# Performance work log

Measured on AMD Instinct MI355X. Metric: run time of the kernel, lower is better.

## Reference

```python
import jax, jax.numpy as jnp
import numpy as np
from jax.ops import segment_sum

N_NODES = 50000
N_EDGES = 800000
N_GRAPHS = 256
F_IN, F_HID, N_HID, N_OUT = 64, 128, 512, 256


def setup_inputs() -> dict:
    key = jax.random.key(0)
    ks = jax.random.split(key, 12)
    x = jax.random.normal(ks[0], (N_NODES, F_IN), dtype=jnp.float32)
    edge_index = jax.random.randint(ks[1], (2, N_EDGES), 0, N_NODES, dtype=jnp.int64)
    batch = jnp.sort(jax.random.randint(ks[2], (N_NODES,), 0, N_GRAPHS, dtype=jnp.int64))
    def lin(k, fan_in, fan_out):
        s = 1.0 / np.sqrt(fan_in)
        return jax.random.uniform(k, (fan_in, fan_out), jnp.float32, -s, s)
    return {
        "x": x, "edge_index": edge_index, "batch": batch,
        "W0": lin(ks[3], F_IN, F_HID), "b0": jnp.zeros((F_HID,), jnp.float32),
        "W1": lin(ks[4], F_HID, F_HID), "b1": jnp.zeros((F_HID,), jnp.float32),
        "W2": lin(ks[5], F_HID, F_HID), "b2": jnp.zeros((F_HID,), jnp.float32),
        "Wm1": lin(ks[6], F_HID, N_HID), "bm1": jnp.zeros((N_HID,), jnp.float32),
        "Wm2": lin(ks[7], N_HID, N_OUT), "bm2": jnp.zeros((N_OUT,), jnp.float32),
    }


def _gcn_norm(edge_index, num_nodes):
    # PyG GCNConv default: add self-loops, symmetric D^{-1/2} A D^{-1/2} norm.
    loop = jnp.arange(num_nodes, dtype=edge_index.dtype)
    src = jnp.concatenate([edge_index[0], loop])
    dst = jnp.concatenate([edge_index[1], loop])
    deg = segment_sum(jnp.ones_like(src, dtype=jnp.float32), dst, num_segments=num_nodes)
    dis = jnp.where(deg > 0, jax.lax.rsqrt(jnp.maximum(deg, 1.0)), 0.0)
    norm = dis[src] * dis[dst]
    return src, dst, norm


def _gcn_conv(x, W, b, src, dst, norm, num_nodes):
    h = x @ W                                  # [N, F_out]
    msg = norm[:, None] * h[src]               # edge-wise gather  [E+N, F_out]
    out = segment_sum(msg, dst, num_segments=num_nodes)  # scatter-add
    return out + b


def reference(x, edge_index, batch, W0, b0, W1, b1, W2, b2, Wm1, bm1, Wm2, bm2):
    n = x.shape[0]
    src, dst, norm = _gcn_norm(edge_index, n)
    h = jax.nn.relu(_gcn_conv(x, W0, b0, src, dst, norm, n))
    h = jax.nn.relu(_gcn_conv(h, W1, b1, src, dst, norm, n))
    h = _gcn_conv(h, W2, b2, src, dst, norm, n)
    # global_mean_pool over graphs
    counts = segment_sum(jnp.ones((n,), jnp.float32), batch, num_segments=N_GRAPHS)
    g = segment_sum(h, batch, num_segments=N_GRAPHS) / jnp.maximum(counts, 1.0)[:, None]
    # mol_mlp: Linear -> ReLU -> Linear
    g = jax.nn.relu(g @ Wm1 + bm1)
    return g @ Wm2 + bm2
```

## Files before the change

kernel.cpp:

```cpp
#include <hip/hip_runtime.h>
#include <hip/hip_bf16.h>
#include <math.h>
#include <stdint.h>

#define N_NODES 50000
#define N_PAD   50048
#define N_EDGES 800000
#define N_GRAPHS 256
#define F_IN 64
#define F_HID 128
#define N_HID 512
#define N_OUT 256

#define NBKT   196
#define BKT_S  6144
#define BKT_CAP 8192
#define EPB    3328
#define NBIN_BLK ((N_EDGES + EPB - 1) / EPB)
#define DUMMY_NODE N_NODES

using bf16x8 = __attribute__((ext_vector_type(8))) short;
using f32x4  = __attribute__((ext_vector_type(4))) float;

__device__ __forceinline__ unsigned int bf16pair(float a, float b) {
    unsigned int ua = __float_as_uint(a);
    unsigned int ub = __float_as_uint(b);
    ua += 0x7fffu + ((ua >> 16) & 1u);
    ub += 0x7fffu + ((ub >> 16) & 1u);
    return (ua >> 16) | (ub & 0xffff0000u);
}
__device__ __forceinline__ unsigned short bf16one(float a) {
    unsigned int ua = __float_as_uint(a);
    ua += 0x7fffu + ((ua >> 16) & 1u);
    return (unsigned short)(ua >> 16);
}
__device__ __forceinline__ float bf16lo(unsigned int u) { return __uint_as_float(u << 16); }
__device__ __forceinline__ float bf16hi(unsigned int u) { return __uint_as_float(u & 0xffff0000u); }

__device__ __forceinline__ void acc8(float* a, uint4 r) {
    a[0] += bf16lo(r.x);  a[1] += bf16hi(r.x);
    a[2] += bf16lo(r.y);  a[3] += bf16hi(r.y);
    a[4] += bf16lo(r.z);  a[5] += bf16hi(r.z);
    a[6] += bf16lo(r.w);  a[7] += bf16hi(r.w);
}

__global__ void cvt_all(const float* __restrict__ in, const float* __restrict__ dis,
                        unsigned int* __restrict__ xb,
                        const float* __restrict__ W0, unsigned short* __restrict__ W0Tb,
                        const float* __restrict__ W1, unsigned short* __restrict__ W1Tb) {
    const int NX = N_NODES * F_IN / 4;
    int idx = blockIdx.x * blockDim.x + threadIdx.x;
    if (idx < NX) {
        int node = idx >> 4;
        float d = dis[node];
        float4 v = ((const float4*)in)[idx];
        ((uint2*)xb)[idx] = make_uint2(bf16pair(d * v.x, d * v.y),
                                       bf16pair(d * v.z, d * v.w));
        if (idx < 16)
            ((uint2*)xb)[(size_t)N_NODES * 16 + idx] = make_uint2(0u, 0u);
    } else {
        int j = idx - NX;
        const int N0 = F_IN * 128;
        const int N1 = F_HID * 128;
        if (j < N0) {
            int k = j >> 7, n = j & 127;
            W0Tb[n * F_IN + k] = bf16one(W0[j]);
        } else if (j < N0 + N1) {
            int jj = j - N0;
            int k = jj >> 7, n = jj & 127;
            W1Tb[n * F_HID + k] = bf16one(W1[jj]);
        }
    }
}

__global__ __launch_bounds__(256) void bin_edges(const int* __restrict__ ei,
                                                 int* __restrict__ bucketCur,
                                                 unsigned int* __restrict__ binned) {
    __shared__ int hist[NBKT];
    __shared__ int lbase[NBKT];
    __shared__ int lcur[NBKT];
    __shared__ int gbase[NBKT];
    __shared__ int scn[256];
    __shared__ unsigned int staging[EPB];
    int tid = threadIdx.x;
    int base = blockIdx.x * EPB;
    int cnt = N_EDGES - base; if (cnt > EPB) cnt = EPB;
    if (tid < NBKT) hist[tid] = 0;
    __syncthreads();
    unsigned int pk[13]; int nk = 0;
#pragma unroll
    for (int u = 0; u < 13; ++u) {
        int e = base + u * 256 + tid;
        if (u * 256 + tid < cnt) {
            unsigned int s = (unsigned int)ei[e];
            unsigned int d = (unsigned int)ei[N_EDGES + e];
            unsigned int b = d >> 8;
            pk[nk++] = (b << 24) | (s << 8) | (d & 255u);
        }
    }
    for (int u = 0; u < nk; ++u) atomicAdd(&hist[pk[u] >> 24], 1);
    __syncthreads();
    int h = (tid < NBKT) ? hist[tid] : 0;
    scn[tid] = h;
    __syncthreads();
    for (int off = 1; off < 256; off <<= 1) {
        int t = (tid >= off) ? scn[tid - off] : 0;
        __syncthreads();
        scn[tid] += t;
        __syncthreads();
    }
    if (tid < NBKT) { int e0 = scn[tid] - h; lbase[tid] = e0; lcur[tid] = e0; }
    __syncthreads();
    for (int u = 0; u < nk; ++u) {
        int pos = atomicAdd(&lcur[pk[u] >> 24], 1);
        staging[pos] = pk[u];
    }
    if (tid < NBKT && hist[tid] > 0)
        gbase[tid] = atomicAdd(&bucketCur[tid], hist[tid]);
    __syncthreads();
    for (int k = tid; k < cnt; k += 256) {
        unsigned int v = staging[k];
        int b = v >> 24;
        binned[(size_t)b * BKT_S + gbase[b] + (k - lbase[b])] = v & 0xffffffu;
    }
}

__global__ __launch_bounds__(256) void deg_scatter(const unsigned int* __restrict__ binned,
                                                   const int* __restrict__ bucketCur,
                                                   int* __restrict__ degs,
                                                   float* __restrict__ dis,
                                                   int* __restrict__ offsets,
                                                   unsigned short* __restrict__ csr) {
    __shared__ int hist[256];
    __shared__ int tsum[256];
    __shared__ int lcur[256];
    __shared__ uint4 scsr4[BKT_CAP / 8];
    unsigned short* scsr = (unsigned short*)scsr4;
    int b = blockIdx.x;
    int tid = threadIdx.x;
    int node0 = b << 8;
    hist[tid] = 0;
    __syncthreads();
    int cnt = bucketCur[b];
    const unsigned int* bb = &binned[(size_t)b * BKT_S];
    for (int k = tid; k < cnt; k += 256)
        atomicAdd(&hist[bb[k] & 255u], 1);
    __syncthreads();
    int d = hist[tid];
    int s = (d + 15) & ~15;
    tsum[tid] = s;
    __syncthreads();
    for (int off = 1; off < 256; off <<= 1) {
        int t = (tid >= off) ? tsum[tid - off] : 0;
        __syncthreads();
        tsum[tid] += t;
        __syncthreads();
    }
    int excl = tsum[tid] - s;
    int tot = tsum[255];
    int csrB = b * BKT_CAP;
    int node = node0 + tid;
    if (node < N_NODES) {
        degs[node] = d;
        dis[node] = rsqrtf((float)(d + 1));
        offsets[node] = csrB + excl;
    }
    lcur[tid] = excl;
    uint2 dv = make_uint2(0xC350C350u, 0xC350C350u);
    for (int k = tid; k < (tot >> 2); k += 256) ((uint2*)scsr)[k] = dv;
    __syncthreads();
    for (int k = tid; k < cnt; k += 256) {
        unsigned int v = bb[k];
        int dl = v & 255u;
        int p = atomicAdd(&lcur[dl], 1);
        scsr[p] = (unsigned short)(v >> 8);
    }
    __syncthreads();
    for (int k = tid; k < (tot >> 3); k += 256)
        ((uint4*)(csr + csrB))[k] = scsr4[k];
}

__global__ __launch_bounds__(256) void gemm01_mfma(const unsigned short* __restrict__ Ab,
                                                   const unsigned short* __restrict__ W0T,
                                                   const float* __restrict__ b0,
                                                   const unsigned short* __restrict__ W1T,
                                                   const float* __restrict__ disv,
                                                   unsigned int* __restrict__ outb, int M) {
    __shared__ unsigned short tile[4][16 * 128];
    int wv = threadIdx.x >> 6;
    int lane = threadIdx.x & 63;
    int m = lane & 15;
    int quad = lane >> 4;
    int row0 = blockIdx.x * 64 + wv * 16;
    char* tl = (char*)&tile[wv][0];
    f32x4 acc[8];
#pragma unroll
    for (int t = 0; t < 8; ++t) acc[t] = (f32x4){0.f, 0.f, 0.f, 0.f};
#pragma unroll
    for (int ks = 0; ks < F_IN; ks += 32) {
        bf16x8 af = *(const bf16x8*)&Ab[(size_t)(row0 + m) * F_IN + ks + quad * 8];
#pragma unroll
        for (int t = 0; t < 8; ++t) {
            bf16x8 bf = *(const bf16x8*)&W0T[(size_t)(t * 16 + m) * F_IN + ks + quad * 8];
            acc[t] = __builtin_amdgcn_mfma_f32_16x16x32_bf16(af, bf, acc[t], 0, 0, 0);
        }
    }
#pragma unroll
    for (int t = 0; t < 8; ++t) {
        int col = t * 16 + m;
        float bcol = b0[col];
#pragma unroll
        for (int r = 0; r < 4; ++r) {
            int row = quad * 4 + r;
            float v = fmaxf(acc[t][r] + bcol, 0.f);
            int byte = (row * 256 + col * 2) ^ ((row & 7) << 4);
            *(unsigned short*)(tl + byte) = bf16one(v);
        }
    }
    __syncthreads();
#pragma unroll
    for (int t = 0; t < 8; ++t) acc[t] = (f32x4){0.f, 0.f, 0.f, 0.f};
#pragma unroll
    for (int ks = 0; ks < F_HID; ks += 32) {
        int byte = (m * 256 + ks * 2 + quad * 16) ^ ((m & 7) << 4);
        bf16x8 af = *(const bf16x8*)(tl + byte);
#pragma unroll
        for (int t = 0; t < 8; ++t) {
            bf16x8 bf = *(const bf16x8*)&W1T[(size_t)(t * 16 + m) * F_HID + ks + quad * 8];
            acc[t] = __builtin_amdgcn_mfma_f32_16x16x32_bf16(af, bf, acc[t], 0, 0, 0);
        }
    }
    float dr[4];
#pragma unroll
    for (int r = 0; r < 4; ++r) {
        int row = row0 + quad * 4 + r;
        dr[r] = (row < M) ? disv[row] : 0.f;
    }
#pragma unroll
    for (int t = 0; t < 8; ++t) {
        int col = t * 16 + m;
#pragma unroll
        for (int r = 0; r < 4; ++r) {
            float v = acc[t][r] * dr[r];
            float vn = __shfl_xor(v, 1, 64);
            if ((m & 1) == 0) {
                int row = row0 + quad * 4 + r;
                outb[(size_t)row * 64 + (col >> 1)] = (row < M) ? bf16pair(v, vn) : 0u;
            }
        }
    }
}

template <bool RELU, bool BIAS, bool SCALEOUT>
__global__ __launch_bounds__(256) void aggregate128b(const uint4* __restrict__ hb4,
                                                     const int* __restrict__ offsets,
                                                     const int* __restrict__ degs,
                                                     const unsigned short* __restrict__ csr,
                                                     const float* __restrict__ dis,
                                                     const float* __restrict__ bias,
                                                     unsigned int* __restrict__ outb) {
    int wave = threadIdx.x >> 6;
    int lane = threadIdx.x & 63;
    int i = blockIdx.x * 4 + wave;
    int sub = lane >> 4;
    int q   = lane & 15;
    if (i >= N_NODES) {
        if (i == N_NODES && sub == 0)
            ((uint4*)outb)[(size_t)N_NODES * 16 + q] = make_uint4(0u, 0u, 0u, 0u);
        return;
    }
    float a[8];
#pragma unroll
    for (int k = 0; k < 8; ++k) a[k] = 0.f;
    int j = offsets[i];
    int e1 = j + ((degs[i] + 15) & ~15);
    for (; j < e1; j += 16) {
        uint2 w = *(const uint2*)&csr[j + 4 * sub];
        int s0 = w.x & 0xffff, s1 = w.x >> 16;
        int s2 = w.y & 0xffff, s3 = w.y >> 16;
        uint4 r0 = hb4[(size_t)s0 * 16 + q];
        uint4 r1 = hb4[(size_t)s1 * 16 + q];
        uint4 r2 = hb4[(size_t)s2 * 16 + q];
        uint4 r3 = hb4[(size_t)s3 * 16 + q];
        acc8(a, r0); acc8(a, r1); acc8(a, r2); acc8(a, r3);
    }
#pragma unroll
    for (int k = 0; k < 8; ++k) a[k] += __shfl_xor(a[k], 16, 64);
#pragma unroll
    for (int k = 0; k < 8; ++k) a[k] += __shfl_xor(a[k], 32, 64);
    uint4 su = hb4[(size_t)i * 16 + q];
    acc8(a, su);
    float dii = dis[i];
#pragma unroll
    for (int k = 0; k < 8; ++k) a[k] *= dii;
    if (BIAS) {
        float4 b0 = ((const float4*)bias)[2 * q];
        float4 b1 = ((const float4*)bias)[2 * q + 1];
        a[0] += b0.x; a[1] += b0.y; a[2] += b0.z; a[3] += b0.w;
        a[4] += b1.x; a[5] += b1.y; a[6] += b1.z; a[7] += b1.w;
    }
    if (RELU) {
#pragma unroll
        for (int k = 0; k < 8; ++k) a[k] = fmaxf(a[k], 0.f);
    }
    if (sub == 0) {
        float sc = SCALEOUT ? dii : 1.f;
        ((uint4*)outb)[(size_t)i * 16 + q] =
            make_uint4(bf16pair(sc * a[0], sc * a[1]), bf16pair(sc * a[2], sc * a[3]),
                       bf16pair(sc * a[4], sc * a[5]), bf16pair(sc * a[6], sc * a[7]));
    }
}

__global__ __launch_bounds__(256) void aggregate_xb(const uint4* __restrict__ xb4,
                                                    const float* __restrict__ x,
                                                    const int* __restrict__ offsets,
                                                    const int* __restrict__ degs,
                                                    const unsigned short* __restrict__ csr,
                                                    const float* __restrict__ dis,
                                                    unsigned int* __restrict__ outb) {
    int wave = threadIdx.x >> 6;
    int lane = threadIdx.x & 63;
    int i = blockIdx.x * 4 + wave;
    int sub = lane >> 3;
    int q   = lane & 7;
    if (i >= N_NODES) {
        if (i == N_NODES && sub == 0)
            ((uint4*)outb)[(size_t)N_NODES * 8 + q] = make_uint4(0u, 0u, 0u, 0u);
        return;
    }
    float a[8];
#pragma unroll
    for (int k = 0; k < 8; ++k) a[k] = 0.f;
    int j = offsets[i];
    int e1 = j + ((degs[i] + 15) & ~15);
    for (; j < e1; j += 16) {
        unsigned int w = *(const unsigned int*)&csr[j + 2 * sub];
        int s0 = w & 0xffff, s1 = w >> 16;
        uint4 r0 = xb4[(size_t)s0 * 8 + q];
        uint4 r1 = xb4[(size_t)s1 * 8 + q];
        acc8(a, r0); acc8(a, r1);
    }
#pragma unroll
    for (int k = 0; k < 8; ++k) a[k] += __shfl_xor(a[k], 8, 64);
#pragma unroll
    for (int k = 0; k < 8; ++k) a[k] += __shfl_xor(a[k], 16, 64);
#pragma unroll
    for (int k = 0; k < 8; ++k) a[k] += __shfl_xor(a[k], 32, 64);
    float dii = dis[i];
    float d2 = dii * dii;
    float4 sx0 = ((const float4*)x)[(size_t)i * 16 + 2 * q];
    float4 sx1 = ((const float4*)x)[(size_t)i * 16 + 2 * q + 1];
    a[0] = dii * a[0] + d2 * sx0.x;  a[1] = dii * a[1] + d2 * sx0.y;
    a[2] = dii * a[2] + d2 * sx0.z;  a[3] = dii * a[3] + d2 * sx0.w;
    a[4] = dii * a[4] + d2 * sx1.x;  a[5] = dii * a[5] + d2 * sx1.y;
    a[6] = dii * a[6] + d2 * sx1.z;  a[7] = dii * a[7] + d2 * sx1.w;
    if (sub == 0)
        ((uint4*)outb)[(size_t)i * 8 + q] =
            make_uint4(bf16pair(a[0], a[1]), bf16pair(a[2], a[3]),
                       bf16pair(a[4], a[5]), bf16pair(a[6], a[7]));
}

__global__ __launch_bounds__(256) void aggregate_pool(const uint4* __restrict__ hb4,
                                                      const int* __restrict__ offsets,
                                                      const int* __restrict__ degs,
                                                      const unsigned short* __restrict__ csr,
                                                      const float* __restrict__ dis,
                                                      const int* __restrict__ batch,
                                                      float* __restrict__ g_acc,
                                                      float* __restrict__ g_cnt) {
    __shared__ float pool[16][128];
    int tid = threadIdx.x;
    int grp = tid >> 4;
    int q   = tid & 15;
    int i = blockIdx.x * 16 + grp;
    float a[8];
#pragma unroll
    for (int k = 0; k < 8; ++k) a[k] = 0.f;
    if (i < N_NODES) {
        int j = offsets[i];
        int e1 = j + ((degs[i] + 15) & ~15);
        for (; j < e1; j += 16) {
            uint4 w0 = *(const uint4*)&csr[j];
            uint4 w1 = *(const uint4*)&csr[j + 8];
            int s[16];
            s[0] = w0.x & 0xffff;  s[1] = w0.x >> 16;
            s[2] = w0.y & 0xffff;  s[3] = w0.y >> 16;
            s[4] = w0.z & 0xffff;  s[5] = w0.z >> 16;
            s[6] = w0.w & 0xffff;  s[7] = w0.w >> 16;
            s[8] = w1.x & 0xffff;  s[9] = w1.x >> 16;
            s[10] = w1.y & 0xffff; s[11] = w1.y >> 16;
            s[12] = w1.z & 0xffff; s[13] = w1.z >> 16;
            s[14] = w1.w & 0xffff; s[15] = w1.w >> 16;
            uint4 r[8];
#pragma unroll
            for (int u = 0; u < 8; ++u) r[u] = hb4[(size_t)s[u] * 16 + q];
#pragma unroll
            for (int u = 0; u < 8; ++u) acc8(a, r[u]);
#pragma unroll
            for (int u = 0; u < 8; ++u) r[u] = hb4[(size_t)s[8 + u] * 16 + q];
#pragma unroll
            for (int u = 0; u < 8; ++u) acc8(a, r[u]);
        }
        uint4 su = hb4[(size_t)i * 16 + q];
        acc8(a, su);
        float dii = dis[i];
#pragma unroll
        for (int k = 0; k < 8; ++k) a[k] *= dii;
    }
#pragma unroll
    for (int k = 0; k < 8; ++k) pool[grp][k * 16 + q] = a[k];
    __syncthreads();
    if (tid < 128) {
        int f = tid;
        int lidx = (f & 7) * 16 + (f >> 3);
        int base = blockIdx.x * 16;
        float acc = 0.f; int cur = -1; float cnt = 0.f;
        for (int n = 0; n < 16; ++n) {
            int i2 = base + n;
            if (i2 >= N_NODES) break;
            int b = batch[i2];
            if (b != cur) {
                if (cur >= 0) {
                    atomicAdd(&g_acc[(size_t)cur * F_HID + f], acc);
                    if (f == 0) atomicAdd(&g_cnt[cur], cnt);
                }
                cur = b; acc = 0.f; cnt = 0.f;
            }
            acc += pool[n][lidx];
            cnt += 1.f;
        }
        if (cur >= 0) {
            atomicAdd(&g_acc[(size_t)cur * F_HID + f], acc);
            if (f == 0) atomicAdd(&g_cnt[cur], cnt);
        }
    }
}

__global__ __launch_bounds__(512) void fused_mlp(const float* __restrict__ g_acc,
                                                 const float* __restrict__ g_cnt,
                                                 const float* __restrict__ W2,
                                                 const float* __restrict__ b2,
                                                 const float* __restrict__ Wm1,
                                                 const float* __restrict__ bm1,
                                                 const float* __restrict__ Wm2,
                                                 const float* __restrict__ bm2,
                                                 float* __restrict__ out) {
    __shared__ float pool_row[F_HID];
    __shared__ float g2row[F_HID];
    __shared__ float hid[N_HID];
    int g = blockIdx.x;
    int t = threadIdx.x;
    if (t < F_HID) {
        float c = g_cnt[g];
        pool_row[t] = g_acc[(size_t)g * F_HID + t] / fmaxf(c, 1.0f);
    }
    __syncthreads();
    if (t < F_HID) {
        float acc = b2[t];
        for (int k = 0; k < F_HID; ++k) acc += pool_row[k] * W2[(size_t)k * F_HID + t];
        g2row[t] = acc;
    }
    __syncthreads();
    {
        float acc = bm1[t];
        for (int k = 0; k < F_HID; ++k) acc += g2row[k] * Wm1[(size_t)k * N_HID + t];
        hid[t] = fmaxf(acc, 0.f);
    }
    __syncthreads();
    if (t < N_OUT) {
        float acc = bm2[t];
        for (int k = 0; k < N_HID; ++k) acc += hid[k] * Wm2[(size_t)k * N_OUT + t];
        out[(size_t)g * N_OUT + t] = acc;
    }
}

extern "C" void kernel_launch(void* const* d_in, const int* in_sizes, int n_in,
                              void* d_out, int out_size, void* d_ws, size_t ws_size,
                              hipStream_t stream) {
    const float* x   = (const float*)d_in[0];
    const int* ei    = (const int*)d_in[1];
    const int* batch = (const int*)d_in[2];
    const float* W0 = (const float*)d_in[3];  const float* b0 = (const float*)d_in[4];
    const float* W1 = (const float*)d_in[5];  const float* b1 = (const float*)d_in[6];
    const float* W2 = (const float*)d_in[7];  const float* b2 = (const float*)d_in[8];
    const float* Wm1 = (const float*)d_in[9];  const float* bm1 = (const float*)d_in[10];
    const float* Wm2 = (const float*)d_in[11]; const float* bm2 = (const float*)d_in[12];

    char* p = (char*)d_ws;
    auto alloc = [&](size_t bytes) -> char* {
        char* r = p;
        p += (bytes + 255) & ~(size_t)255;
        return r;
    };
    int*   bucketCur = (int*)alloc(NBKT * 4);
    float* g_acc  = (float*)alloc((size_t)N_GRAPHS * F_HID * 4);
    float* g_cnt  = (float*)alloc(N_GRAPHS * 4);
    size_t zero_bytes = (size_t)(p - (char*)bucketCur);
    unsigned int* binned = (unsigned int*)alloc((size_t)NBKT * BKT_S * 4);
    int*   offsets = (int*)alloc((size_t)N_NODES * 4);
    int*   degs    = (int*)alloc((size_t)N_NODES * 4);
    float* dis     = (float*)alloc((size_t)N_NODES * 4);
    unsigned short* csr = (unsigned short*)alloc((size_t)NBKT * BKT_CAP * 2 + 32);
    unsigned int* xb     = (unsigned int*)alloc((size_t)N_PAD * F_IN / 2 * 4);
    unsigned int* axb    = (unsigned int*)alloc((size_t)N_PAD * F_IN / 2 * 4);
    unsigned int* h_tmpb = (unsigned int*)alloc((size_t)N_PAD * F_HID / 2 * 4);
    unsigned int* h_bb   = (unsigned int*)alloc((size_t)N_PAD * F_HID / 2 * 4);
    unsigned short* W0Tb = (unsigned short*)alloc((size_t)128 * F_IN * 2);
    unsigned short* W1Tb = (unsigned short*)alloc((size_t)128 * F_HID * 2);
    (void)ws_size; (void)in_sizes; (void)n_in; (void)out_size;

    (void)hipMemsetAsync(bucketCur, 0, zero_bytes, stream);

    bin_edges<<<NBIN_BLK, 256, 0, stream>>>(ei, bucketCur, binned);
    deg_scatter<<<NBKT, 256, 0, stream>>>(binned, bucketCur, degs, dis, offsets, csr);

    const int NCVT = N_NODES * F_IN / 4 + (F_IN + F_HID) * 128;
    cvt_all<<<(NCVT + 255) / 256, 256, 0, stream>>>(x, dis, xb, W0, W0Tb, W1, W1Tb);

    int agg_grid = N_NODES / 4 + 1;
    int mfma_grid = N_PAD / 64;

    aggregate_xb<<<agg_grid, 256, 0, stream>>>((const uint4*)xb, x, offsets, degs, csr, dis, axb);
    gemm01_mfma<<<mfma_grid, 256, 0, stream>>>(
        (const unsigned short*)axb, W0Tb, b0, W1Tb, dis, h_tmpb, N_NODES);
    aggregate128b<true, true, true><<<agg_grid, 256, 0, stream>>>(
        (const uint4*)h_tmpb, offsets, degs, csr, dis, b1, h_bb);
    aggregate_pool<<<(N_NODES + 15) / 16, 256, 0, stream>>>(
        (const uint4*)h_bb, offsets, degs, csr, dis, batch, g_acc, g_cnt);

    fused_mlp<<<N_GRAPHS, 512, 0, stream>>>(g_acc, g_cnt, W2, b2, Wm1, bm1, Wm2, bm2,
                                            (float*)d_out);
}
```

Measured before the change: 248.2 us.

## Fuse first-layer aggregation into MFMA GEMM and regroup aggregation threads per node

Layer-0 neighbor aggregation now runs inside the GEMM kernel. Each block aggregates its 64 rows into a swizzled LDS tile and feeds the MFMA directly, which removes the axb intermediate buffer and one launch. The 128-wide aggregation kernel now gives each node a 16-lane group that walks all 16 CSR entries per iteration, instead of splitting edges across a wave and reducing with shuffles. This trades cross-lane reductions for more serial gather work per thread. The fused kernel runs only 782 blocks, so the aggregation phase may have less parallelism to hide gather latency.

```diff
diff --git a/kernel.cpp b/kernel.cpp
--- a/kernel.cpp
+++ b/kernel.cpp
@@ -42,6 +42,19 @@
     a[2] += bf16lo(r.y);  a[3] += bf16hi(r.y);
     a[4] += bf16lo(r.z);  a[5] += bf16hi(r.z);
     a[6] += bf16lo(r.w);  a[7] += bf16hi(r.w);
+}
+
+__device__ __forceinline__ void csr16(const unsigned short* __restrict__ csr, int j, int* s) {
+    uint4 w0 = *(const uint4*)&csr[j];
+    uint4 w1 = *(const uint4*)&csr[j + 8];
+    s[0] = w0.x & 0xffff;  s[1] = w0.x >> 16;
+    s[2] = w0.y & 0xffff;  s[3] = w0.y >> 16;
+    s[4] = w0.z & 0xffff;  s[5] = w0.z >> 16;
+    s[6] = w0.w & 0xffff;  s[7] = w0.w >> 16;
+    s[8] = w1.x & 0xffff;  s[9] = w1.x >> 16;
+    s[10] = w1.y & 0xffff; s[11] = w1.y >> 16;
+    s[12] = w1.z & 0xffff; s[13] = w1.z >> 16;
+    s[14] = w1.w & 0xffff; s[15] = w1.w >> 16;
 }
 
 __global__ void cvt_all(const float* __restrict__ in, const float* __restrict__ dis,
@@ -180,25 +193,76 @@
         ((uint4*)(csr + csrB))[k] = scsr4[k];
 }
 
-__global__ __launch_bounds__(256) void gemm01_mfma(const unsigned short* __restrict__ Ab,
-                                                   const unsigned short* __restrict__ W0T,
-                                                   const float* __restrict__ b0,
-                                                   const unsigned short* __restrict__ W1T,
-                                                   const float* __restrict__ disv,
-                                                   unsigned int* __restrict__ outb, int M) {
+__global__ __launch_bounds__(256) void agg_gemm01(const uint4* __restrict__ xb4,
+                                                  const float* __restrict__ x,
+                                                  const int* __restrict__ offsets,
+                                                  const int* __restrict__ degs,
+                                                  const unsigned short* __restrict__ csr,
+                                                  const float* __restrict__ dis,
+                                                  const unsigned short* __restrict__ W0T,
+                                                  const float* __restrict__ b0,
+                                                  const unsigned short* __restrict__ W1T,
+                                                  unsigned int* __restrict__ outb, int M) {
+    __shared__ unsigned short atile[64 * 64];
     __shared__ unsigned short tile[4][16 * 128];
-    int wv = threadIdx.x >> 6;
-    int lane = threadIdx.x & 63;
+    int tid = threadIdx.x;
+    int row0 = blockIdx.x * 64;
+    char* at = (char*)atile;
+    {
+        int grp = tid >> 3;
+        int q   = tid & 7;
+#pragma unroll
+        for (int pass = 0; pass < 2; ++pass) {
+            int node = grp + pass * 32;
+            int i = row0 + node;
+            float a[8];
+#pragma unroll
+            for (int k = 0; k < 8; ++k) a[k] = 0.f;
+            if (i < N_NODES) {
+                int j = offsets[i];
+                int e1 = j + ((degs[i] + 15) & ~15);
+                for (; j < e1; j += 16) {
+                    int s[16];
+                    csr16(csr, j, s);
+                    uint4 r[8];
+#pragma unroll
+                    for (int u = 0; u < 8; ++u) r[u] = xb4[(size_t)s[u] * 8 + q];
+#pragma unroll
+                    for (int u = 0; u < 8; ++u) acc8(a, r[u]);
+#pragma unroll
+                    for (int u = 0; u < 8; ++u) r[u] = xb4[(size_t)s[8 + u] * 8 + q];
+#pragma unroll
+                    for (int u = 0; u < 8; ++u) acc8(a, r[u]);
+                }
+                float dii = dis[i];
+                float d2 = dii * dii;
+                float4 sx0 = ((const float4*)x)[(size_t)i * 16 + 2 * q];
+                float4 sx1 = ((const float4*)x)[(size_t)i * 16 + 2 * q + 1];
+                a[0] = dii * a[0] + d2 * sx0.x;  a[1] = dii * a[1] + d2 * sx0.y;
+                a[2] = dii * a[2] + d2 * sx0.z;  a[3] = dii * a[3] + d2 * sx0.w;
+                a[4] = dii * a[4] + d2 * sx1.x;  a[5] = dii * a[5] + d2 * sx1.y;
+                a[6] = dii * a[6] + d2 * sx1.z;  a[7] = dii * a[7] + d2 * sx1.w;
+            }
+            int byte = (node * 128 + q * 16) ^ ((node & 7) << 4);
+            *(uint4*)(at + byte) =
+                make_uint4(bf16pair(a[0], a[1]), bf16pair(a[2], a[3]),
+                           bf16pair(a[4], a[5]), bf16pair(a[6], a[7]));
+        }
+    }
+    __syncthreads();
+    int wv = tid >> 6;
+    int lane = tid & 63;
     int m = lane & 15;
     int quad = lane >> 4;
-    int row0 = blockIdx.x * 64 + wv * 16;
+    int wrow0 = row0 + wv * 16;
     char* tl = (char*)&tile[wv][0];
     f32x4 acc[8];
 #pragma unroll
     for (int t = 0; t < 8; ++t) acc[t] = (f32x4){0.f, 0.f, 0.f, 0.f};
 #pragma unroll
     for (int ks = 0; ks < F_IN; ks += 32) {
-        bf16x8 af = *(const bf16x8*)&Ab[(size_t)(row0 + m) * F_IN + ks + quad * 8];
+        int abyte = ((wv * 16 + m) * 128 + (ks + quad * 8) * 2) ^ ((m & 7) << 4);
+        bf16x8 af = *(const bf16x8*)(at + abyte);
 #pragma unroll
         for (int t = 0; t < 8; ++t) {
             bf16x8 bf = *(const bf16x8*)&W0T[(size_t)(t * 16 + m) * F_IN + ks + quad * 8];
@@ -233,8 +297,8 @@
     float dr[4];
 #pragma unroll
     for (int r = 0; r < 4; ++r) {
-        int row = row0 + quad * 4 + r;
-        dr[r] = (row < M) ? disv[row] : 0.f;
+        int row = wrow0 + quad * 4 + r;
+        dr[r] = (row < M) ? dis[row] : 0.f;
     }
 #pragma unroll
     for (int t = 0; t < 8; ++t) {
@@ -244,7 +308,7 @@
             float v = acc[t][r] * dr[r];
             float vn = __shfl_xor(v, 1, 64);
             if ((m & 1) == 0) {
-                int row = row0 + quad * 4 + r;
+                int row = wrow0 + quad * 4 + r;
                 outb[(size_t)row * 64 + (col >> 1)] = (row < M) ? bf16pair(v, vn) : 0u;
             }
         }
@@ -252,20 +316,19 @@
 }
 
 template <bool RELU, bool BIAS, bool SCALEOUT>
-__global__ __launch_bounds__(256) void aggregate128b(const uint4* __restrict__ hb4,
+__global__ __launch_bounds__(256) void aggregate128g(const uint4* __restrict__ hb4,
                                                      const int* __restrict__ offsets,
                                                      const int* __restrict__ degs,
                                                      const unsigned short* __restrict__ csr,
                                                      const float* __restrict__ dis,
                                                      const float* __restrict__ bias,
                                                      unsigned int* __restrict__ outb) {
-    int wave = threadIdx.x >> 6;
-    int lane = threadIdx.x & 63;
-    int i = blockIdx.x * 4 + wave;
-    int sub = lane >> 4;
-    int q   = lane & 15;
+    int tid = threadIdx.x;
+    int grp = tid >> 4;
+    int q   = tid & 15;
+    int i = blockIdx.x * 16 + grp;
     if (i >= N_NODES) {
-        if (i == N_NODES && sub == 0)
+        if (i == N_NODES)
             ((uint4*)outb)[(size_t)N_NODES * 16 + q] = make_uint4(0u, 0u, 0u, 0u);
         return;
     }
@@ -275,19 +338,18 @@
     int j = offsets[i];
     int e1 = j + ((degs[i] + 15) & ~15);
     for (; j < e1; j += 16) {
-        uint2 w = *(const uint2*)&csr[j + 4 * sub];
-        int s0 = w.x & 0xffff, s1 = w.x >> 16;
-        int s2 = w.y & 0xffff, s3 = w.y >> 16;
-        uint4 r0 = hb4[(size_t)s0 * 16 + q];
-        uint4 r1 = hb4[(size_t)s1 * 16 + q];
-        uint4 r2 = hb4[(size_t)s2 * 16 + q];
-        uint4 r3 = hb4[(size_t)s3 * 16 + q];
-        acc8(a, r0); acc8(a, r1); acc8(a, r2); acc8(a, r3);
-    }
-#pragma unroll
-    for (int k = 0; k < 8; ++k) a[k] += __shfl_xor(a[k], 16, 64);
-#pragma unroll
-    for (int k = 0; k < 8; ++k) a[k] += __shfl_xor(a[k], 32, 64);
+        int s[16];
+        csr16(csr, j, s);
+        uint4 r[8];
+#pragma unroll
+        for (int u = 0; u < 8; ++u) r[u] = hb4[(size_t)s[u] * 16 + q];
+#pragma unroll
+        for (int u = 0; u < 8; ++u) acc8(a, r[u]);
+#pragma unroll
+        for (int u = 0; u < 8; ++u) r[u] = hb4[(size_t)s[8 + u] * 16 + q];
+#pragma unroll
+        for (int u = 0; u < 8; ++u) acc8(a, r[u]);
+    }
     uint4 su = hb4[(size_t)i * 16 + q];
     acc8(a, su);
     float dii = dis[i];
@@ -303,61 +365,10 @@
 #pragma unroll
         for (int k = 0; k < 8; ++k) a[k] = fmaxf(a[k], 0.f);
     }
-    if (sub == 0) {
-        float sc = SCALEOUT ? dii : 1.f;
-        ((uint4*)outb)[(size_t)i * 16 + q] =
-            make_uint4(bf16pair(sc * a[0], sc * a[1]), bf16pair(sc * a[2], sc * a[3]),
-                       bf16pair(sc * a[4], sc * a[5]), bf16pair(sc * a[6], sc * a[7]));
-    }
-}
-
-__global__ __launch_bounds__(256) void aggregate_xb(const uint4* __restrict__ xb4,
-                                                    const float* __restrict__ x,
-                                                    const int* __restrict__ offsets,
-                                                    const int* __restrict__ degs,
-                                                    const unsigned short* __restrict__ csr,
-                                                    const float* __restrict__ dis,
-                                                    unsigned int* __restrict__ outb) {
-    int wave = threadIdx.x >> 6;
-    int lane = threadIdx.x & 63;
-    int i = blockIdx.x * 4 + wave;
-    int sub = lane >> 3;
-    int q   = lane & 7;
-    if (i >= N_NODES) {
-        if (i == N_NODES && sub == 0)
-            ((uint4*)outb)[(size_t)N_NODES * 8 + q] = make_uint4(0u, 0u, 0u, 0u);
-        return;
-    }
-    float a[8];
-#pragma unroll
-    for (int k = 0; k < 8; ++k) a[k] = 0.f;
-    int j = offsets[i];
-    int e1 = j + ((degs[i] + 15) & ~15);
-    for (; j < e1; j += 16) {
-        unsigned int w = *(const unsigned int*)&csr[j + 2 * sub];
-        int s0 = w & 0xffff, s1 = w >> 16;
-        uint4 r0 = xb4[(size_t)s0 * 8 + q];
-        uint4 r1 = xb4[(size_t)s1 * 8 + q];
-        acc8(a, r0); acc8(a, r1);
-    }
-#pragma unroll
-    for (int k = 0; k < 8; ++k) a[k] += __shfl_xor(a[k], 8, 64);
-#pragma unroll
-    for (int k = 0; k < 8; ++k) a[k] += __shfl_xor(a[k], 16, 64);
-#pragma unroll
-    for (int k = 0; k < 8; ++k) a[k] += __shfl_xor(a[k], 32, 64);
-    float dii = dis[i];
-    float d2 = dii * dii;
-    float4 sx0 = ((const float4*)x)[(size_t)i * 16 + 2 * q];
-    float4 sx1 = ((const float4*)x)[(size_t)i * 16 + 2 * q + 1];
-    a[0] = dii * a[0] + d2 * sx0.x;  a[1] = dii * a[1] + d2 * sx0.y;
-    a[2] = dii * a[2] + d2 * sx0.z;  a[3] = dii * a[3] + d2 * sx0.w;
-    a[4] = dii * a[4] + d2 * sx1.x;  a[5] = dii * a[5] + d2 * sx1.y;
-    a[6] = dii * a[6] + d2 * sx1.z;  a[7] = dii * a[7] + d2 * sx1.w;
-    if (sub == 0)
-        ((uint4*)outb)[(size_t)i * 8 + q] =
-            make_uint4(bf16pair(a[0], a[1]), bf16pair(a[2], a[3]),
-                       bf16pair(a[4], a[5]), bf16pair(a[6], a[7]));
+    float sc = SCALEOUT ? dii : 1.f;
+    ((uint4*)outb)[(size_t)i * 16 + q] =
+        make_uint4(bf16pair(sc * a[0], sc * a[1]), bf16pair(sc * a[2], sc * a[3]),
+                   bf16pair(sc * a[4], sc * a[5]), bf16pair(sc * a[6], sc * a[7]));
 }
 
 __global__ __launch_bounds__(256) void aggregate_pool(const uint4* __restrict__ hb4,
@@ -380,17 +391,8 @@
         int j = offsets[i];
         int e1 = j + ((degs[i] + 15) & ~15);
         for (; j < e1; j += 16) {
-            uint4 w0 = *(const uint4*)&csr[j];
-            uint4 w1 = *(const uint4*)&csr[j + 8];
             int s[16];
-            s[0] = w0.x & 0xffff;  s[1] = w0.x >> 16;
-            s[2] = w0.y & 0xffff;  s[3] = w0.y >> 16;
-            s[4] = w0.z & 0xffff;  s[5] = w0.z >> 16;
-            s[6] = w0.w & 0xffff;  s[7] = w0.w >> 16;
-            s[8] = w1.x & 0xffff;  s[9] = w1.x >> 16;
-            s[10] = w1.y & 0xffff; s[11] = w1.y >> 16;
-            s[12] = w1.z & 0xffff; s[13] = w1.z >> 16;
-            s[14] = w1.w & 0xffff; s[15] = w1.w >> 16;
+            csr16(csr, j, s);
             uint4 r[8];
 #pragma unroll
             for (int u = 0; u < 8; ++u) r[u] = hb4[(size_t)s[u] * 16 + q];
@@ -502,7 +504,6 @@
     float* dis     = (float*)alloc((size_t)N_NODES * 4);
     unsigned short* csr = (unsigned short*)alloc((size_t)NBKT * BKT_CAP * 2 + 32);
     unsigned int* xb     = (unsigned int*)alloc((size_t)N_PAD * F_IN / 2 * 4);
-    unsigned int* axb    = (unsigned int*)alloc((size_t)N_PAD * F_IN / 2 * 4);
     unsigned int* h_tmpb = (unsigned int*)alloc((size_t)N_PAD * F_HID / 2 * 4);
     unsigned int* h_bb   = (unsigned int*)alloc((size_t)N_PAD * F_HID / 2 * 4);
     unsigned short* W0Tb = (unsigned short*)alloc((size_t)128 * F_IN * 2);
@@ -517,15 +518,16 @@
     const int NCVT = N_NODES * F_IN / 4 + (F_IN + F_HID) * 128;
     cvt_all<<<(NCVT + 255) / 256, 256, 0, stream>>>(x, dis, xb, W0, W0Tb, W1, W1Tb);
 
-    int agg_grid = N_NODES / 4 + 1;
     int mfma_grid = N_PAD / 64;
-
-    aggregate_xb<<<agg_grid, 256, 0, stream>>>((const uint4*)xb, x, offsets, degs, csr, dis, axb);
-    gemm01_mfma<<<mfma_grid, 256, 0, stream>>>(
-        (const unsigned short*)axb, W0Tb, b0, W1Tb, dis, h_tmpb, N_NODES);
-    aggregate128b<true, true, true><<<agg_grid, 256, 0, stream>>>(
+    int agg16_grid = N_NODES / 16 + 1;
+    int pool_grid = (N_NODES + 15) / 16;
+
+    agg_gemm01<<<mfma_grid, 256, 0, stream>>>(
+        (const uint4*)xb, x, offsets, degs, csr, dis,
+        W0Tb, b0, W1Tb, h_tmpb, N_NODES);
+    aggregate128g<true, true, true><<<agg16_grid, 256, 0, stream>>>(
         (const uint4*)h_tmpb, offsets, degs, csr, dis, b1, h_bb);
-    aggregate_pool<<<(N_NODES + 15) / 16, 256, 0, stream>>>(
+    aggregate_pool<<<pool_grid, 256, 0, stream>>>(
         (const uint4*)h_bb, offsets, degs, csr, dis, batch, g_acc, g_cnt);
 
     fused_mlp<<<N_GRAPHS, 512, 0, stream>>>(g_acc, g_cnt, W2, b2, Wm1, bm1, Wm2, bm2,
```

New measurement: 239.7 us. -3.4%, faster.
